# Performance work log

Hardware: AMD Instinct MI355X
Metric: run time of the kernel (lower is better)

Reference implementation:

```python
import jax, jax.numpy as jnp
import numpy as np

DEC_HIDDEN = 512


def setup_inputs() -> dict:
    key = jax.random.key(0)
    k1, k2, k3, k4 = jax.random.split(key, 4)
    B, S, DEC, ENC2 = 32, 2048, 512, 1024
    s = jax.random.normal(k1, (1, B, DEC), dtype=jnp.float32)
    enc_output = jax.random.normal(k2, (B, S, ENC2), dtype=jnp.float32)
    # nn.Linear weights: attn [dec_hidden, enc_hidden*2 + dec_hidden], v [1, dec_hidden]
    W_attn = jax.random.normal(k3, (DEC, DEC + ENC2), dtype=jnp.float32) * (1.0 / np.sqrt(DEC + ENC2))
    W_v = jax.random.normal(k4, (1, DEC), dtype=jnp.float32) * (1.0 / np.sqrt(DEC))
    return {"s": s, "enc_output": enc_output, "W_attn": W_attn, "W_v": W_v}


def reference(s, enc_output, W_attn, W_v):
    # s: [1, B, D] -> [B, D]; enc_output: [B, S, 2E]
    s = jnp.squeeze(s, axis=0)
    dec = s.shape[-1]
    # torch.cat((s_repeated, enc_output), dim=2) @ W_attn.T, computed without
    # materializing the repeat/concat: split W_attn by column blocks.
    W_s = W_attn[:, :dec]       # [D, D]   (columns matching s)
    W_e = W_attn[:, dec:]       # [D, 2E]  (columns matching enc_output)
    # energy: [B, S, D]
    energy = jnp.tanh(
        jnp.einsum('bd,hd->bh', s, W_s)[:, None, :]
        + jnp.einsum('bse,he->bsh', enc_output, W_e)
    )
    # atten: [B, S]
    atten = jnp.einsum('bsh,h->bs', energy, W_v[0])
    soft_attn_weights = jax.nn.softmax(atten, axis=1)
    # context: [B, 2E]
    context = jnp.einsum('bs,bse->be', soft_attn_weights, enc_output)
    return (context, soft_attn_weights)
```

## Files before the change

kernel.cpp:

```cpp
#include <hip/hip_runtime.h>
#include <hip/hip_bf16.h>


typedef __attribute__((ext_vector_type(8))) short bf16x8;
typedef __attribute__((ext_vector_type(4))) float f32x4;
typedef __attribute__((address_space(3))) unsigned lds_u32;
typedef const __attribute__((address_space(1))) unsigned g_u32;

#define SB0() __builtin_amdgcn_sched_barrier(0)

static __device__ __forceinline__ unsigned short f2bf(float f) {
    union { float f; unsigned u; } v; v.f = f;
    unsigned r = (v.u + 0x7fffu + ((v.u >> 16) & 1u)) >> 16;
    return (unsigned short)r;
}

static __device__ __forceinline__ unsigned pk2(float x, float y) {
    union { __hip_bfloat162 h; unsigned u; } c;
    c.h = __float22bfloat162_rn(make_float2(x, y));
    return c.u;
}

static __device__ __forceinline__ float fast_tanh(float x) {
    return 1.0f - 2.0f / (__expf(2.0f * x) + 1.0f);
}

__global__ __launch_bounds__(256) void prep_sw(const float* __restrict__ s,
                                               const float* __restrict__ Wat,
                                               float* __restrict__ sW) {
    int id = blockIdx.x * 256 + threadIdx.x;
    int b = id >> 9, h = id & 511;
    const float4* wr = (const float4*)(Wat + (size_t)h * 1536);
    const float4* sr = (const float4*)(s + (size_t)b * 512);
    float acc = 0.f;
#pragma unroll 8
    for (int i = 0; i < 128; ++i) {
        float4 w = wr[i], sv = sr[i];
        acc += w.x * sv.x + w.y * sv.y + w.z * sv.z + w.w * sv.w;
    }
    sW[id] = acc;
}

__global__ __launch_bounds__(256) void prep_weB(const float* __restrict__ Wat,
                                                unsigned short* __restrict__ WebfB) {
    int tid = blockIdx.x * 256 + threadIdx.x;
    int lane = tid & 63;
    int g = tid >> 6;
    int nf = g & 3, kk = (g >> 2) & 1, i = (g >> 3) & 15, w = g >> 7;
    int col = w * 64 + nf * 16 + (lane & 15);
    int k0 = i * 64 + kk * 32 + (lane >> 4) * 8;
    const float* src = Wat + (size_t)col * 1536 + 512 + k0;
    float4 w0 = *(const float4*)src;
    float4 w1 = *(const float4*)(src + 4);
    union { unsigned short us[8]; int4 v; } p;
    p.us[0] = f2bf(w0.x); p.us[1] = f2bf(w0.y); p.us[2] = f2bf(w0.z); p.us[3] = f2bf(w0.w);
    p.us[4] = f2bf(w1.x); p.us[5] = f2bf(w1.y); p.us[6] = f2bf(w1.z); p.us[7] = f2bf(w1.w);
    *(int4*)(WebfB + (size_t)tid * 8) = p.v;
}

__global__ __launch_bounds__(256, 2) void energy_kernel(
    const float* __restrict__ enc, const unsigned short* __restrict__ WebfB,
    const float* __restrict__ sW, const float* __restrict__ Wv,
    float* __restrict__ atten) {
    __shared__ __align__(16) float lA[3][4096];
    __shared__ float lred[4][64];

    const int t = threadIdx.x;
    const int lane = t & 63;
    const int wave = t >> 6;
    const int bid = blockIdx.x;
    const int m0 = (bid & 1023) * 64;
    const int nh = bid >> 10;
    const int b = m0 >> 11;
    const int l15 = lane & 15;
    const int lkg = lane >> 4;
    const int cg = nh * 4 + wave;
    const int n0 = cg * 64;

    const float* gsrc[4];
    int ldoff[4];
#pragma unroll
    for (int q = 0; q < 4; ++q) {
        int rq = wave * 16 + q * 4 + lkg;
        int cl = l15 ^ (rq & 7);
        gsrc[q] = enc + (size_t)(m0 + rq) * 1024 + cl * 4;
        ldoff[q] = (wave * 16 + q * 4) * 64;
    }

    const unsigned short* wB = WebfB + (size_t)cg * 65536 + lane * 8;

    f32x4 acc[4][4];
#pragma unroll
    for (int mf = 0; mf < 4; ++mf)
#pragma unroll
        for (int nf = 0; nf < 4; ++nf) acc[mf][nf] = (f32x4){0.f, 0.f, 0.f, 0.f};

    auto stage = [&](int step, float* buf) {
#pragma unroll
        for (int q = 0; q < 4; ++q)
            __builtin_amdgcn_global_load_lds((g_u32*)(gsrc[q] + step * 64),
                                             (lds_u32*)(buf + ldoff[q]), 16, 0, 0);
    };
    auto loadB = [&](int step, bf16x8* bf) {
#pragma unroll
        for (int kk = 0; kk < 2; ++kk)
#pragma unroll
            for (int nf = 0; nf < 4; ++nf)
                bf[kk * 4 + nf] = *(const bf16x8*)(wB + (((step * 2 + kk) * 4 + nf) << 9));
    };
    auto compute = [&](const float* lbuf, const bf16x8* bf) {
#pragma unroll
        for (int kk = 0; kk < 2; ++kk) {
            const int c0 = kk * 8 + lkg * 2;
#pragma unroll
            for (int mf = 0; mf < 4; ++mf) {
                const int r = mf * 16 + l15;
                const int r7 = r & 7;
                float4 a0 = *(const float4*)&lbuf[r * 64 + ((c0 ^ r7) << 2)];
                float4 a1 = *(const float4*)&lbuf[r * 64 + (((c0 + 1) ^ r7) << 2)];
                union { unsigned u[4]; bf16x8 v; } af;
                af.u[0] = pk2(a0.x, a0.y); af.u[1] = pk2(a0.z, a0.w);
                af.u[2] = pk2(a1.x, a1.y); af.u[3] = pk2(a1.z, a1.w);
#pragma unroll
                for (int nf = 0; nf < 4; ++nf)
                    acc[mf][nf] = __builtin_amdgcn_mfma_f32_16x16x32_bf16(
                        af.v, bf[kk * 4 + nf], acc[mf][nf], 0, 0, 0);
            }
        }
    };

    float* p0 = (float*)lA[0];
    float* p1 = (float*)lA[1];
    float* p2 = (float*)lA[2];
    bf16x8 bA[8], bB[8];

    stage(0, p0);
    loadB(0, bA);
    stage(1, p1);

#pragma unroll 1
    for (int k = 0; k < 7; ++k) {
        const int i = 2 * k;
        asm volatile("s_waitcnt vmcnt(12)" ::: "memory");
        SB0();
        __builtin_amdgcn_s_barrier();
        loadB(i + 1, bB);
        SB0();
        stage(i + 2, p2);
        SB0();
        compute(p0, bA);
        { float* tp = p0; p0 = p1; p1 = p2; p2 = tp; }
        asm volatile("s_waitcnt vmcnt(12)" ::: "memory");
        SB0();
        __builtin_amdgcn_s_barrier();
        loadB(i + 2, bA);
        SB0();
        stage(i + 3, p2);
        SB0();
        compute(p0, bB);
        { float* tp = p0; p0 = p1; p1 = p2; p2 = tp; }
    }
    asm volatile("s_waitcnt vmcnt(12)" ::: "memory");
    SB0();
    __builtin_amdgcn_s_barrier();
    loadB(15, bB);
    SB0();
    compute(p0, bA);
    { float* tp = p0; p0 = p1; p1 = p2; p2 = tp; }
    asm volatile("s_waitcnt vmcnt(8)" ::: "memory");
    SB0();
    __builtin_amdgcn_s_barrier();
    compute(p0, bB);

    float sWv[4], wvv[4];
#pragma unroll
    for (int nf = 0; nf < 4; ++nf) {
        int col = n0 + nf * 16 + l15;
        sWv[nf] = sW[(b << 9) + col];
        wvv[nf] = Wv[col];
    }
    float pa[4][4];
#pragma unroll
    for (int mf = 0; mf < 4; ++mf) {
#pragma unroll
        for (int r = 0; r < 4; ++r) pa[mf][r] = 0.f;
#pragma unroll
        for (int nf = 0; nf < 4; ++nf)
#pragma unroll
            for (int r = 0; r < 4; ++r)
                pa[mf][r] += fast_tanh(acc[mf][nf][r] + sWv[nf]) * wvv[nf];
    }
#pragma unroll
    for (int m = 1; m < 16; m <<= 1)
#pragma unroll
        for (int mf = 0; mf < 4; ++mf)
#pragma unroll
            for (int r = 0; r < 4; ++r)
                pa[mf][r] += __shfl_xor(pa[mf][r], m, 64);

    if (l15 == 0) {
#pragma unroll
        for (int mf = 0; mf < 4; ++mf)
#pragma unroll
            for (int r = 0; r < 4; ++r)
                lred[wave][mf * 16 + lkg * 4 + r] = pa[mf][r];
    }
    __syncthreads();
    if (t < 64) {
        float ssum = lred[0][t] + lred[1][t] + lred[2][t] + lred[3][t];
        atomicAdd(&atten[m0 + t], ssum);
    }
}

__global__ __launch_bounds__(256) void zero_atten(float* __restrict__ atten) {
    atten[blockIdx.x * 256 + threadIdx.x] = 0.f;
}

__global__ __launch_bounds__(256) void softmax_kernel(const float* __restrict__ atten,
                                                      float* __restrict__ out) {
    int b = blockIdx.x, t = threadIdx.x;
    const float* row = atten + b * 2048;
    float v[8];
#pragma unroll
    for (int i = 0; i < 8; ++i) v[i] = row[t + 256 * i];
    float mx = v[0];
#pragma unroll
    for (int i = 1; i < 8; ++i) mx = fmaxf(mx, v[i]);
#pragma unroll
    for (int m = 1; m < 64; m <<= 1) mx = fmaxf(mx, __shfl_xor(mx, m, 64));
    __shared__ float redm[4], reds[4];
    if ((t & 63) == 0) redm[t >> 6] = mx;
    __syncthreads();
    mx = fmaxf(fmaxf(redm[0], redm[1]), fmaxf(redm[2], redm[3]));
    float sum = 0.f;
#pragma unroll
    for (int i = 0; i < 8; ++i) { v[i] = __expf(v[i] - mx); sum += v[i]; }
#pragma unroll
    for (int m = 1; m < 64; m <<= 1) sum += __shfl_xor(sum, m, 64);
    if ((t & 63) == 0) reds[t >> 6] = sum;
    __syncthreads();
    sum = reds[0] + reds[1] + reds[2] + reds[3];
    float inv = 1.0f / sum;
    float* soft = out + 32768;
#pragma unroll
    for (int i = 0; i < 8; ++i) soft[b * 2048 + t + 256 * i] = v[i] * inv;
}

__global__ __launch_bounds__(256) void ctx_partial(const float* __restrict__ enc,
                                                   const float* __restrict__ soft,
                                                   float* __restrict__ part) {
    int blk = blockIdx.x;
    int b = blk >> 5, s0 = (blk & 31) * 64;
    int t = threadIdx.x;
    float4 a = {0.f, 0.f, 0.f, 0.f};
    const float* base = enc + ((size_t)(b * 2048 + s0)) * 1024 + t * 4;
    const float* sw = soft + b * 2048 + s0;
#pragma unroll 4
    for (int s = 0; s < 64; ++s) {
        float w = sw[s];
        float4 e = *(const float4*)(base + (size_t)s * 1024);
        a.x += w * e.x; a.y += w * e.y; a.z += w * e.z; a.w += w * e.w;
    }
    *(float4*)(part + (size_t)blk * 1024 + t * 4) = a;
}

__global__ __launch_bounds__(256) void ctx_reduce(const float* __restrict__ part,
                                                  float* __restrict__ ctx) {
    int id = blockIdx.x * 256 + threadIdx.x;
    int b = id >> 10, e = id & 1023;
    float s = 0.f;
#pragma unroll 8
    for (int c = 0; c < 32; ++c) s += part[((size_t)(b * 32 + c)) * 1024 + e];
    ctx[id] = s;
}

extern "C" void kernel_launch(void* const* d_in, const int* in_sizes, int n_in,
                              void* d_out, int out_size, void* d_ws, size_t ws_size,
                              hipStream_t stream) {
    const float* s   = (const float*)d_in[0];
    const float* enc = (const float*)d_in[1];
    const float* Wat = (const float*)d_in[2];
    const float* Wv  = (const float*)d_in[3];
    float* out = (float*)d_out;

    char* ws = (char*)d_ws;
    float* sW             = (float*)ws;
    unsigned short* WebfB = (unsigned short*)(ws + (64 << 10));
    float* atten          = (float*)(ws + (64 << 10) + (1 << 20));
    float* part           = (float*)(ws + (64 << 10) + (1 << 20) + (256 << 10));

    prep_sw<<<64, 256, 0, stream>>>(s, Wat, sW);
    prep_weB<<<256, 256, 0, stream>>>(Wat, WebfB);
    zero_atten<<<256, 256, 0, stream>>>(atten);
    energy_kernel<<<2048, 256, 0, stream>>>(enc, WebfB, sW, Wv, atten);
    softmax_kernel<<<32, 256, 0, stream>>>(atten, out);
    ctx_partial<<<1024, 256, 0, stream>>>(enc, out + 32768, part);
    ctx_reduce<<<128, 256, 0, stream>>>(part, out);
}
```

Baseline: 195.9 us.

## Retile energy GEMM to 128x256 blocks with 2x2 wave grid and K=32 steps

```diff
diff --git a/kernel.cpp b/kernel.cpp
--- a/kernel.cpp
+++ b/kernel.cpp
@@ -46,9 +46,9 @@
     int tid = blockIdx.x * 256 + threadIdx.x;
     int lane = tid & 63;
     int g = tid >> 6;
-    int nf = g & 3, kk = (g >> 2) & 1, i = (g >> 3) & 15, w = g >> 7;
-    int col = w * 64 + nf * 16 + (lane & 15);
-    int k0 = i * 64 + kk * 32 + (lane >> 4) * 8;
+    int nf = g & 7, step = (g >> 3) & 31, cg = g >> 8;
+    int col = cg * 128 + nf * 16 + (lane & 15);
+    int k0 = step * 32 + (lane >> 4) * 8;
     const float* src = Wat + (size_t)col * 1536 + 512 + k0;
     float4 w0 = *(const float4*)src;
     float4 w1 = *(const float4*)(src + 4);
@@ -58,6 +58,10 @@
     *(int4*)(WebfB + (size_t)tid * 8) = p.v;
 }
 
+__global__ __launch_bounds__(256) void zero_atten(float* __restrict__ atten) {
+    atten[blockIdx.x * 256 + threadIdx.x] = 0.f;
+}
+
 __global__ __launch_bounds__(256, 2) void energy_kernel(
     const float* __restrict__ enc, const unsigned short* __restrict__ WebfB,
     const float* __restrict__ sW, const float* __restrict__ Wv,
@@ -68,64 +72,63 @@
     const int t = threadIdx.x;
     const int lane = t & 63;
     const int wave = t >> 6;
+    const int rg = wave >> 1;
+    const int cgw = wave & 1;
     const int bid = blockIdx.x;
-    const int m0 = (bid & 1023) * 64;
-    const int nh = bid >> 10;
+    const int rt = ((bid >> 4) << 3) | (bid & 7);
+    const int ch = (bid >> 3) & 1;
+    const int m0 = rt * 128;
     const int b = m0 >> 11;
     const int l15 = lane & 15;
     const int lkg = lane >> 4;
-    const int cg = nh * 4 + wave;
-    const int n0 = cg * 64;
+    const int cgAll = ch * 2 + cgw;
+    const int colbase = cgAll * 128;
 
     const float* gsrc[4];
     int ldoff[4];
 #pragma unroll
     for (int q = 0; q < 4; ++q) {
-        int rq = wave * 16 + q * 4 + lkg;
-        int cl = l15 ^ (rq & 7);
-        gsrc[q] = enc + (size_t)(m0 + rq) * 1024 + cl * 4;
-        ldoff[q] = (wave * 16 + q * 4) * 64;
-    }
-
-    const unsigned short* wB = WebfB + (size_t)cg * 65536 + lane * 8;
-
-    f32x4 acc[4][4];
+        int s = q * 256 + t;
+        int row_s = s >> 3;
+        int chs = (s & 7) ^ (row_s & 7);
+        gsrc[q] = enc + (size_t)(m0 + row_s) * 1024 + chs * 4;
+        ldoff[q] = (q * 256 + wave * 64) * 4;
+    }
+
+    const unsigned short* wB = WebfB + (size_t)cgAll * 131072 + lane * 8;
+
+    f32x4 acc[4][8];
 #pragma unroll
     for (int mf = 0; mf < 4; ++mf)
 #pragma unroll
-        for (int nf = 0; nf < 4; ++nf) acc[mf][nf] = (f32x4){0.f, 0.f, 0.f, 0.f};
+        for (int nf = 0; nf < 8; ++nf) acc[mf][nf] = (f32x4){0.f, 0.f, 0.f, 0.f};
 
     auto stage = [&](int step, float* buf) {
 #pragma unroll
         for (int q = 0; q < 4; ++q)
-            __builtin_amdgcn_global_load_lds((g_u32*)(gsrc[q] + step * 64),
+            __builtin_amdgcn_global_load_lds((g_u32*)(gsrc[q] + step * 32),
                                              (lds_u32*)(buf + ldoff[q]), 16, 0, 0);
     };
     auto loadB = [&](int step, bf16x8* bf) {
 #pragma unroll
-        for (int kk = 0; kk < 2; ++kk)
-#pragma unroll
-            for (int nf = 0; nf < 4; ++nf)
-                bf[kk * 4 + nf] = *(const bf16x8*)(wB + (((step * 2 + kk) * 4 + nf) << 9));
+        for (int nf = 0; nf < 8; ++nf)
+            bf[nf] = *(const bf16x8*)(wB + (((size_t)step * 8 + nf) << 9));
     };
     auto compute = [&](const float* lbuf, const bf16x8* bf) {
 #pragma unroll
-        for (int kk = 0; kk < 2; ++kk) {
-            const int c0 = kk * 8 + lkg * 2;
-#pragma unroll
-            for (int mf = 0; mf < 4; ++mf) {
-                const int r = mf * 16 + l15;
-                const int r7 = r & 7;
-                float4 a0 = *(const float4*)&lbuf[r * 64 + ((c0 ^ r7) << 2)];
-                float4 a1 = *(const float4*)&lbuf[r * 64 + (((c0 + 1) ^ r7) << 2)];
-                union { unsigned u[4]; bf16x8 v; } af;
-                af.u[0] = pk2(a0.x, a0.y); af.u[1] = pk2(a0.z, a0.w);
-                af.u[2] = pk2(a1.x, a1.y); af.u[3] = pk2(a1.z, a1.w);
-#pragma unroll
-                for (int nf = 0; nf < 4; ++nf)
-                    acc[mf][nf] = __builtin_amdgcn_mfma_f32_16x16x32_bf16(
-                        af.v, bf[kk * 4 + nf], acc[mf][nf], 0, 0, 0);
-            }
+        for (int mf = 0; mf < 4; ++mf) {
+            const int r = rg * 64 + mf * 16 + l15;
+            const int r7 = r & 7;
+            const int c0 = lkg * 2;
+            float4 a0 = *(const float4*)&lbuf[r * 32 + ((c0 ^ r7) << 2)];
+            float4 a1 = *(const float4*)&lbuf[r * 32 + (((c0 + 1) ^ r7) << 2)];
+            union { unsigned u[4]; bf16x8 v; } af;
+            af.u[0] = pk2(a0.x, a0.y); af.u[1] = pk2(a0.z, a0.w);
+            af.u[2] = pk2(a1.x, a1.y); af.u[3] = pk2(a1.z, a1.w);
+#pragma unroll
+            for (int nf = 0; nf < 8; ++nf)
+                acc[mf][nf] = __builtin_amdgcn_mfma_f32_16x16x32_bf16(
+                    af.v, bf[nf], acc[mf][nf], 0, 0, 0);
         }
     };
 
@@ -139,7 +142,7 @@
     stage(1, p1);
 
 #pragma unroll 1
-    for (int k = 0; k < 7; ++k) {
+    for (int k = 0; k < 15; ++k) {
         const int i = 2 * k;
         asm volatile("s_waitcnt vmcnt(12)" ::: "memory");
         SB0();
@@ -163,7 +166,7 @@
     asm volatile("s_waitcnt vmcnt(12)" ::: "memory");
     SB0();
     __builtin_amdgcn_s_barrier();
-    loadB(15, bB);
+    loadB(31, bB);
     SB0();
     compute(p0, bA);
     { float* tp = p0; p0 = p1; p1 = p2; p2 = tp; }
@@ -172,10 +175,10 @@
     __builtin_amdgcn_s_barrier();
     compute(p0, bB);
 
-    float sWv[4], wvv[4];
-#pragma unroll
-    for (int nf = 0; nf < 4; ++nf) {
-        int col = n0 + nf * 16 + l15;
+    float sWv[8], wvv[8];
+#pragma unroll
+    for (int nf = 0; nf < 8; ++nf) {
+        int col = colbase + nf * 16 + l15;
         sWv[nf] = sW[(b << 9) + col];
         wvv[nf] = Wv[col];
     }
@@ -185,7 +188,7 @@
 #pragma unroll
         for (int r = 0; r < 4; ++r) pa[mf][r] = 0.f;
 #pragma unroll
-        for (int nf = 0; nf < 4; ++nf)
+        for (int nf = 0; nf < 8; ++nf)
 #pragma unroll
             for (int r = 0; r < 4; ++r)
                 pa[mf][r] += fast_tanh(acc[mf][nf][r] + sWv[nf]) * wvv[nf];
@@ -206,14 +209,11 @@
                 lred[wave][mf * 16 + lkg * 4 + r] = pa[mf][r];
     }
     __syncthreads();
-    if (t < 64) {
-        float ssum = lred[0][t] + lred[1][t] + lred[2][t] + lred[3][t];
+    if (t < 128) {
+        int rgw = t >> 6, lsub = t & 63;
+        float ssum = lred[rgw * 2 + 0][lsub] + lred[rgw * 2 + 1][lsub];
         atomicAdd(&atten[m0 + t], ssum);
     }
-}
-
-__global__ __launch_bounds__(256) void zero_atten(float* __restrict__ atten) {
-    atten[blockIdx.x * 256 + threadIdx.x] = 0.f;
 }
 
 __global__ __launch_bounds__(256) void softmax_kernel(const float* __restrict__ atten,
@@ -292,7 +292,7 @@
     prep_sw<<<64, 256, 0, stream>>>(s, Wat, sW);
     prep_weB<<<256, 256, 0, stream>>>(Wat, WebfB);
     zero_atten<<<256, 256, 0, stream>>>(atten);
-    energy_kernel<<<2048, 256, 0, stream>>>(enc, WebfB, sW, Wv, atten);
+    energy_kernel<<<1024, 256, 0, stream>>>(enc, WebfB, sW, Wv, atten);
     softmax_kernel<<<32, 256, 0, stream>>>(atten, out);
     ctx_partial<<<1024, 256, 0, stream>>>(enc, out + 32768, part);
     ctx_reduce<<<128, 256, 0, stream>>>(part, out);
```

New measurement: 180.2 us. 1.09x faster.
